# Kernel tuning notes

Measured on AMD Instinct MI355X. Metric: run time of the kernel, lower is better.

The kernel has to match this reference:

```python
import jax, jax.numpy as jnp
import numpy as np

B, L, C, H, D2 = 1, 384, 256, 8, 128
d = C // H
EPS = 1e-5
SCALE = 1.0 / np.sqrt(d).astype(np.float32)


def setup_inputs() -> dict:
    key = jax.random.key(0)
    ks = jax.random.split(key, 20)

    def lin(k, fin, fout):
        return (jax.random.normal(k, (fin, fout), jnp.float32) / np.sqrt(fin)).astype(jnp.float32)

    return {
        "x2d": jax.random.normal(ks[0], (B, L, L, D2), jnp.float32),
        "x3d": jax.random.normal(ks[1], (B, L, C), jnp.float32),
        "Wq": lin(ks[2], C, C), "bq": jax.random.normal(ks[3], (C,), jnp.float32) * 0.02,
        "Wk": lin(ks[4], C, C), "bk": jax.random.normal(ks[5], (C,), jnp.float32) * 0.02,
        "Wv": lin(ks[6], C, C), "bv": jax.random.normal(ks[7], (C,), jnp.float32) * 0.02,
        "Wpre": lin(ks[8], D2, C), "bpre": jax.random.normal(ks[9], (C,), jnp.float32) * 0.02,
        "ln_g": jnp.ones((C,), jnp.float32), "ln_b": jnp.zeros((C,), jnp.float32),
        "Weq": lin(ks[10], C, C), "beq": jax.random.normal(ks[11], (C,), jnp.float32) * 0.02,
        "Wek": lin(ks[12], C, C), "bek": jax.random.normal(ks[13], (C,), jnp.float32) * 0.02,
        "Wo": lin(ks[14], C, C), "bo": jax.random.normal(ks[15], (C,), jnp.float32) * 0.02,
    }


def reference(x2d, x3d, Wq, bq, Wk, bk, Wv, bv, Wpre, bpre, ln_g, ln_b,
              Weq, beq, Wek, bek, Wo, bo):
    def heads(x):  # (B,L,C) -> (B,H,L,d)
        return x.reshape(B, L, H, d).transpose(0, 2, 1, 3)

    q = heads(x3d @ Wq + bq)
    k = heads(x3d @ Wk + bk)
    v = heads(x3d @ Wv + bv)

    # pre_proj: Linear -> LayerNorm -> ReLU on pair features
    e = x2d @ Wpre + bpre                              # (B,L,L,C)
    mu = jnp.mean(e, axis=-1, keepdims=True)
    var = jnp.mean((e - mu) ** 2, axis=-1, keepdims=True)
    e = jax.nn.relu((e - mu) * jax.lax.rsqrt(var + EPS) * ln_g + ln_b)

    efq = (e @ Weq + beq).reshape(B, L, L, H, d)       # efq[b,i,j,h,:]
    efk = (e @ Wek + bek).reshape(B, L, L, H, d)

    # scores[b,h,i,j] = q_i.k_j + sum_d efk[b,i,j,h,d]*q[b,h,j,d], then scale
    scores = jnp.einsum('bhid,bhjd->bhij', q, k) \
           + jnp.einsum('bijhd,bhjd->bhij', efk, q)
    scores = scores * SCALE

    w = jax.nn.softmax(scores, axis=-1)
    x1 = jnp.einsum('bhij,bhjd->bhid', w, v)
    # x2[b,h,i,d] = sum_j scores[b,h,i,j] * efq[b,i,j,h,d]
    x2 = jnp.einsum('bhij,bijhd->bhid', scores, efq)

    x = (x1 + x2).transpose(0, 2, 1, 3).reshape(B, L, C)
    return x @ Wo + bo
```

## Files before the change

kernel.cpp:

```cpp
#include <hip/hip_runtime.h>
#include <hip/hip_bf16.h>

#define LLEN 384
#define CDIM 256
#define NH 8
#define HD 32
#define DIN 128
#define LN_EPS 1e-5f
#define SCL 0.17677669529663687f

typedef __attribute__((ext_vector_type(8))) short bh8;
typedef __attribute__((ext_vector_type(4))) float f32x4;
typedef __attribute__((ext_vector_type(4))) unsigned int u32x4;

__device__ __forceinline__ unsigned short f2bf(float f){
  unsigned int u = __float_as_uint(f);
  u += 0x7fffu + ((u >> 16) & 1u);
  return (unsigned short)(u >> 16);
}

__device__ __forceinline__ float pk_reduce8(const float* v, int lane){
  bool b0 = lane & 1, b1 = lane & 2, b2 = lane & 4;
  float r0 = (b0 ? v[1] : v[0]) + __shfl_xor(b0 ? v[0] : v[1], 1, 64);
  float r1 = (b0 ? v[3] : v[2]) + __shfl_xor(b0 ? v[2] : v[3], 1, 64);
  float r2 = (b0 ? v[5] : v[4]) + __shfl_xor(b0 ? v[4] : v[5], 1, 64);
  float r3 = (b0 ? v[7] : v[6]) + __shfl_xor(b0 ? v[6] : v[7], 1, 64);
  float s0 = (b1 ? r1 : r0) + __shfl_xor(b1 ? r0 : r1, 2, 64);
  float s1 = (b1 ? r3 : r2) + __shfl_xor(b1 ? r2 : r3, 2, 64);
  float t0 = (b2 ? s1 : s0) + __shfl_xor(b2 ? s0 : s1, 4, 64);
  return t0 + __shfl_xor(t0, 8, 64);
}

__global__ __launch_bounds__(256) void pack_w(
    const float* __restrict__ Wpre, const float* __restrict__ Weq,
    const float* __restrict__ Wek,  const float* __restrict__ Wq,
    const float* __restrict__ Wk,   const float* __restrict__ Wv,
    unsigned short* __restrict__ Pp, unsigned short* __restrict__ Pq,
    unsigned short* __restrict__ Pk, unsigned short* __restrict__ PWq,
    unsigned short* __restrict__ PWk, unsigned short* __restrict__ PWv)
{
  int tid = blockIdx.x * 256 + threadIdx.x;
  const float* W; unsigned short* P; int base;
  if      (tid <  4096){ W = Wpre; P = Pp;  base = tid;         }
  else if (tid < 12288){ W = Weq;  P = Pq;  base = tid -  4096; }
  else if (tid < 20480){ W = Wek;  P = Pk;  base = tid - 12288; }
  else if (tid < 28672){ W = Wq;   P = PWq; base = tid - 20480; }
  else if (tid < 36864){ W = Wk;   P = PWk; base = tid - 28672; }
  else                 { W = Wv;   P = PWv; base = tid - 36864; }
  int l   = base & 63;
  int c   = (base >> 6) & 15;
  int kc  = base >> 10;
  int krow = kc*32 + (l >> 4)*8;
  int col  = c*16 + (l & 15);
  unsigned int wds[4];
  #pragma unroll
  for (int p = 0; p < 4; p++){
    unsigned short lo = f2bf(W[(size_t)(krow + 2*p    )*CDIM + col]);
    unsigned short hi = f2bf(W[(size_t)(krow + 2*p + 1)*CDIM + col]);
    wds[p] = (unsigned int)lo | ((unsigned int)hi << 16);
  }
  uint4 v; v.x = wds[0]; v.y = wds[1]; v.z = wds[2]; v.w = wds[3];
  *(uint4*)(P + (size_t)base*8) = v;
}

__global__ __launch_bounds__(256) void qkv_mfma(
    const float* __restrict__ x3d,
    const float* __restrict__ bq, const float* __restrict__ bk, const float* __restrict__ bv,
    const unsigned short* __restrict__ PWq, const unsigned short* __restrict__ PWk,
    const unsigned short* __restrict__ PWv,
    float* __restrict__ Vm, unsigned short* __restrict__ QmH,
    float* __restrict__ QmT, unsigned short* __restrict__ PKt)
{
  __shared__ __align__(16) unsigned short Xb[64*264];
  const int bx = blockIdx.x;
  const int jb = bx / 3, m = bx % 3;
  const int t  = threadIdx.x;
  const int w  = t >> 6, l = t & 63, q4 = l >> 4, lm = l & 15;
  const int wbase = w << 6;

  const float* src = x3d + (size_t)jb*64*CDIM;
  #pragma unroll
  for (int it = 0; it < 16; it++){
    int idx = it*256 + t;
    int r = idx >> 6, k4 = (idx & 63) << 2;
    float4 v = *(const float4*)(src + (size_t)r*CDIM + k4);
    ushort4 b;
    b.x = f2bf(v.x); b.y = f2bf(v.y); b.z = f2bf(v.z); b.w = f2bf(v.w);
    *(ushort4*)(&Xb[r*264 + k4]) = b;
  }
  __syncthreads();

  const unsigned short* P = (m == 0) ? PWq : (m == 1) ? PWk : PWv;
  const float* bias       = (m == 0) ? bq  : (m == 1) ? bk  : bv;
  f32x4 acc[4][4];
  #pragma unroll
  for (int a = 0; a < 4; a++)
    #pragma unroll
    for (int b = 0; b < 4; b++){ f32x4 z = {0.f,0.f,0.f,0.f}; acc[a][b] = z; }
  #pragma unroll
  for (int kc = 0; kc < 8; kc++){
    bh8 af[4];
    #pragma unroll
    for (int rt = 0; rt < 4; rt++)
      af[rt] = *(const bh8*)(&Xb[(rt*16 + lm)*264 + kc*32 + q4*8]);
    #pragma unroll
    for (int ct = 0; ct < 4; ct++){
      bh8 bf = *(const bh8*)(P + ((size_t)(kc*16 + (w*4 + ct))*64 + l)*8);
      #pragma unroll
      for (int rt = 0; rt < 4; rt++)
        acc[rt][ct] = __builtin_amdgcn_mfma_f32_16x16x32_bf16(af[rt], bf, acc[rt][ct], 0, 0, 0);
    }
  }
  #pragma unroll
  for (int ct = 0; ct < 4; ct++){
    int c = wbase + ct*16 + lm;
    float bb = bias[c];
    #pragma unroll
    for (int rt = 0; rt < 4; rt++)
      #pragma unroll
      for (int rg = 0; rg < 4; rg++){
        int row = jb*64 + rt*16 + q4*4 + rg;
        float v = acc[rt][ct][rg] + bb;
        if (m == 0){
          QmH[(size_t)row*CDIM + c] = f2bf(v);
          QmT[(size_t)c*LLEN + row] = v;
        } else if (m == 1){
          int kc2 = c >> 5;
          int jj2 = c & 7;
          int l2  = ((c >> 3) & 3)*16 + (row & 15);
          PKt[(((size_t)kc2*24 + (row >> 4))*64 + l2)*8 + jj2] = f2bf(v);
        } else {
          Vm[(size_t)row*CDIM + c] = v;
        }
      }
  }
}

__global__ __launch_bounds__(256, 3) void x3d_tiles(
  const float* __restrict__ x2d,
  const float* __restrict__ bpre, const float* __restrict__ ln_g, const float* __restrict__ ln_b,
  const float* __restrict__ beq,  const float* __restrict__ bek,
  const float* __restrict__ QmT,  const unsigned short* __restrict__ QmH,
  const unsigned short* __restrict__ PKt,
  const unsigned short* __restrict__ Pp, const unsigned short* __restrict__ Pq,
  const unsigned short* __restrict__ Pk,
  float* __restrict__ Sg, float* __restrict__ x2part)
{
  __shared__ __align__(16) unsigned short EX[64*264];
  __shared__ float rowstat[4][64][2];
  __shared__ float muS[64], istdS[64];
  __shared__ float bpreS[CDIM], gS[CDIM], bSh[CDIM], beqS[CDIM], bekS[CDIM];
  __shared__ float qk1S[NH*64];

  const int bx = blockIdx.x;
  const int i = bx / 6, jt = bx % 6, j0 = jt * 64;
  const int t = threadIdx.x;
  const int w = t >> 6, l = t & 63, q4 = l >> 4, lm = l & 15;
  const int wbase = w << 6;

  {
    #pragma unroll
    for (int hh = 0; hh < 2; hh++){
      int h = 2*w + hh;
      bh8 aq = *(const bh8*)(QmH + (size_t)i*CDIM + h*HD + q4*8);
      #pragma unroll
      for (int ct = 0; ct < 4; ct++){
        bh8 bf = *(const bh8*)(PKt + (((size_t)h*24 + (jt*4 + ct))*64 + l)*8);
        f32x4 z = {0.f,0.f,0.f,0.f};
        f32x4 a1 = __builtin_amdgcn_mfma_f32_16x16x32_bf16(aq, bf, z, 0, 0, 0);
        if (q4 == 0) qk1S[h*64 + ct*16 + lm] = a1[0];
      }
    }
  }

  bpreS[t] = bpre[t]; gS[t] = ln_g[t]; bSh[t] = ln_b[t];
  beqS[t]  = beq[t];  bekS[t] = bek[t];

  {
    const float* src = x2d + ((size_t)i*LLEN + j0)*DIN;
    #pragma unroll
    for (int it = 0; it < 8; it++){
      int r  = it*8 + (t >> 5);
      int k4 = (t & 31)*4;
      u32x4 uv = __builtin_nontemporal_load((const u32x4*)(src + (size_t)r*DIN + k4));
      ushort4 b;
      b.x = f2bf(__uint_as_float(uv.x)); b.y = f2bf(__uint_as_float(uv.y));
      b.z = f2bf(__uint_as_float(uv.z)); b.w = f2bf(__uint_as_float(uv.w));
      *(ushort4*)(&EX[r*136 + k4]) = b;
    }
  }
  __syncthreads();

  f32x4 acc[4][4];
  #pragma unroll
  for (int a = 0; a < 4; a++)
    #pragma unroll
    for (int b = 0; b < 4; b++){ f32x4 z = {0.f,0.f,0.f,0.f}; acc[a][b] = z; }
  #pragma unroll
  for (int kc = 0; kc < 4; kc++){
    bh8 af[4];
    #pragma unroll
    for (int rt = 0; rt < 4; rt++)
      af[rt] = *(const bh8*)(&EX[(rt*16 + lm)*136 + kc*32 + q4*8]);
    #pragma unroll
    for (int ct = 0; ct < 4; ct++){
      bh8 bf = *(const bh8*)(Pp + ((size_t)(kc*16 + (w*4 + ct))*64 + l)*8);
      #pragma unroll
      for (int rt = 0; rt < 4; rt++)
        acc[rt][ct] = __builtin_amdgcn_mfma_f32_16x16x32_bf16(af[rt], bf, acc[rt][ct], 0, 0, 0);
    }
  }

  #pragma unroll
  for (int rt = 0; rt < 4; rt++){
    float v[8];
    #pragma unroll
    for (int p = 0; p < 8; p++) v[p] = 0.f;
    #pragma unroll
    for (int ct = 0; ct < 4; ct++){
      float bb = bpreS[wbase + ct*16 + lm];
      #pragma unroll
      for (int rg = 0; rg < 4; rg++){
        float x = acc[rt][ct][rg] + bb;
        acc[rt][ct][rg] = x;
        v[2*rg]   += x;
        v[2*rg+1] += x*x;
      }
    }
    float red = pk_reduce8(v, lm);
    if (lm < 8){
      int p = lm;
      rowstat[w][rt*16 + q4*4 + (p >> 1)][p & 1] = red;
    }
  }
  __syncthreads();
  if (t < 64){
    float s  = rowstat[0][t][0] + rowstat[1][t][0] + rowstat[2][t][0] + rowstat[3][t][0];
    float s2 = rowstat[0][t][1] + rowstat[1][t][1] + rowstat[2][t][1] + rowstat[3][t][1];
    float mu = s * (1.f/256.f);
    float var = s2 * (1.f/256.f) - mu*mu;
    muS[t] = mu;
    istdS[t] = rsqrtf(var + LN_EPS);
  }
  __syncthreads();

  #pragma unroll
  for (int rt = 0; rt < 4; rt++){
    #pragma unroll
    for (int rg = 0; rg < 4; rg++){
      int row = rt*16 + q4*4 + rg;
      float mu = muS[row], is = istdS[row];
      #pragma unroll
      for (int ct = 0; ct < 4; ct++){
        int c = wbase + ct*16 + lm;
        float v = (acc[rt][ct][rg] - mu)*is*gS[c] + bSh[c];
        v = fmaxf(v, 0.f);
        EX[row*264 + c] = f2bf(v);
      }
    }
  }
  __syncthreads();

  #pragma unroll
  for (int a = 0; a < 4; a++)
    #pragma unroll
    for (int b = 0; b < 4; b++){ f32x4 z = {0.f,0.f,0.f,0.f}; acc[a][b] = z; }
  #pragma unroll
  for (int kc = 0; kc < 8; kc++){
    bh8 af[4];
    #pragma unroll
    for (int rt = 0; rt < 4; rt++)
      af[rt] = *(const bh8*)(&EX[(rt*16 + lm)*264 + kc*32 + q4*8]);
    #pragma unroll
    for (int ct = 0; ct < 4; ct++){
      bh8 bf = *(const bh8*)(Pk + ((size_t)(kc*16 + (w*4 + ct))*64 + l)*8);
      #pragma unroll
      for (int rt = 0; rt < 4; rt++)
        acc[rt][ct] = __builtin_amdgcn_mfma_f32_16x16x32_bf16(af[rt], bf, acc[rt][ct], 0, 0, 0);
    }
  }

  float screg[4];
  #pragma unroll
  for (int rt = 0; rt < 4; rt++){
    float v[8];
    #pragma unroll
    for (int p = 0; p < 8; p++) v[p] = 0.f;
    #pragma unroll
    for (int ct = 0; ct < 4; ct++){
      int c = wbase + ct*16 + lm;
      float bek_ = bekS[c];
      float4 qv = *(const float4*)(QmT + (size_t)c*LLEN + j0 + rt*16 + q4*4);
      int wh = ct >> 1;
      v[0 + wh] += (acc[rt][ct][0] + bek_) * qv.x;
      v[2 + wh] += (acc[rt][ct][1] + bek_) * qv.y;
      v[4 + wh] += (acc[rt][ct][2] + bek_) * qv.z;
      v[6 + wh] += (acc[rt][ct][3] + bek_) * qv.w;
    }
    float red = pk_reduce8(v, lm);
    int p = lm & 7;
    int jloc = rt*16 + q4*4 + (p >> 1);
    float sc = (red + qk1S[(2*w + (p & 1))*64 + jloc]) * SCL;
    screg[rt] = sc;
    if (lm < 8)
      Sg[((size_t)i*NH + 2*w + (p & 1))*LLEN + j0 + jloc] = sc;
  }

  #pragma unroll
  for (int a = 0; a < 4; a++)
    #pragma unroll
    for (int b = 0; b < 4; b++){ f32x4 z = {0.f,0.f,0.f,0.f}; acc[a][b] = z; }
  #pragma unroll
  for (int kc = 0; kc < 8; kc++){
    bh8 af[4];
    #pragma unroll
    for (int rt = 0; rt < 4; rt++)
      af[rt] = *(const bh8*)(&EX[(rt*16 + lm)*264 + kc*32 + q4*8]);
    #pragma unroll
    for (int ct = 0; ct < 4; ct++){
      bh8 bf = *(const bh8*)(Pq + ((size_t)(kc*16 + (w*4 + ct))*64 + l)*8);
      #pragma unroll
      for (int rt = 0; rt < 4; rt++)
        acc[rt][ct] = __builtin_amdgcn_mfma_f32_16x16x32_bf16(af[rt], bf, acc[rt][ct], 0, 0, 0);
    }
  }

  float x2p[4] = {0.f, 0.f, 0.f, 0.f};
  float bq4[4];
  #pragma unroll
  for (int ct = 0; ct < 4; ct++) bq4[ct] = beqS[wbase + ct*16 + lm];
  #pragma unroll
  for (int rt = 0; rt < 4; rt++){
    float sb[8];
    #pragma unroll
    for (int p = 0; p < 8; p++)
      sb[p] = __shfl(screg[rt], (l & 48) | p, 64);
    #pragma unroll
    for (int ct = 0; ct < 4; ct++){
      int wh = ct >> 1;
      #pragma unroll
      for (int rg = 0; rg < 4; rg++)
        x2p[ct] = fmaf(sb[2*rg + wh], acc[rt][ct][rg] + bq4[ct], x2p[ct]);
    }
  }
  {
    bool b4 = l & 16, b5 = l & 32;
    float r0 = (b4 ? x2p[1] : x2p[0]) + __shfl_xor(b4 ? x2p[0] : x2p[1], 16, 64);
    float r1 = (b4 ? x2p[3] : x2p[2]) + __shfl_xor(b4 ? x2p[2] : x2p[3], 16, 64);
    float q  = (b5 ? r1 : r0) + __shfl_xor(b5 ? r0 : r1, 32, 64);
    int ctq = ((l >> 4) & 1) | (((l >> 5) & 1) << 1);
    x2part[((size_t)jt*LLEN + i)*CDIM + wbase + ctq*16 + lm] = q;
  }
}

__global__ __launch_bounds__(256) void finish(
    const float* __restrict__ Sg, const float* __restrict__ x2part,
    const float* __restrict__ Vm, const float* __restrict__ Wo,
    const float* __restrict__ bo, float* __restrict__ out)
{
  __shared__ float scoresS[NH*LLEN];
  __shared__ float xoutS[CDIM];
  const int i = blockIdx.x;
  const int t = threadIdx.x;

  #pragma unroll
  for (int it = 0; it < 3; it++)
    ((float4*)scoresS)[it*256 + t] = ((const float4*)(Sg + (size_t)i*NH*LLEN))[it*256 + t];
  __syncthreads();

  const int h = t >> 5;
  const int g32 = t & 31;
  float sv[12];
  float mx = -3.0e38f;
  #pragma unroll
  for (int it = 0; it < 12; it++){
    float s = scoresS[h*LLEN + it*32 + g32];
    sv[it] = s;
    mx = fmaxf(mx, s);
  }
  #pragma unroll
  for (int mk = 1; mk < 32; mk <<= 1) mx = fmaxf(mx, __shfl_xor(mx, mk, 64));
  float den = 0.f;
  #pragma unroll
  for (int it = 0; it < 12; it++){ float e = __expf(sv[it] - mx); sv[it] = e; den += e; }
  #pragma unroll
  for (int mk = 1; mk < 32; mk <<= 1) den += __shfl_xor(den, mk, 64);
  float rden = 1.f / den;
  #pragma unroll
  for (int it = 0; it < 12; it++) scoresS[h*LLEN + it*32 + g32] = sv[it]*rden;
  __syncthreads();

  float a0 = 0.f, a1 = 0.f, a2 = 0.f, a3 = 0.f;
  {
    const float* vp = Vm + t;
    const float* sp = scoresS + h*LLEN;
    #pragma unroll 4
    for (int j = 0; j < LLEN; j += 4){
      a0 = fmaf(sp[j+0], vp[(size_t)(j+0)*CDIM], a0);
      a1 = fmaf(sp[j+1], vp[(size_t)(j+1)*CDIM], a1);
      a2 = fmaf(sp[j+2], vp[(size_t)(j+2)*CDIM], a2);
      a3 = fmaf(sp[j+3], vp[(size_t)(j+3)*CDIM], a3);
    }
  }
  float x2v = 0.f;
  #pragma unroll
  for (int jt = 0; jt < 6; jt++)
    x2v += x2part[((size_t)jt*LLEN + i)*CDIM + t];
  xoutS[t] = (a0 + a1) + (a2 + a3) + x2v;
  __syncthreads();

  float b0a = bo[t], b1a = 0.f, b2a = 0.f, b3a = 0.f;
  #pragma unroll 4
  for (int c = 0; c < CDIM; c += 4){
    b0a = fmaf(xoutS[c+0], Wo[(size_t)(c+0)*CDIM + t], b0a);
    b1a = fmaf(xoutS[c+1], Wo[(size_t)(c+1)*CDIM + t], b1a);
    b2a = fmaf(xoutS[c+2], Wo[(size_t)(c+2)*CDIM + t], b2a);
    b3a = fmaf(xoutS[c+3], Wo[(size_t)(c+3)*CDIM + t], b3a);
  }
  out[(size_t)i*CDIM + t] = (b0a + b1a) + (b2a + b3a);
}

extern "C" void kernel_launch(void* const* d_in, const int* in_sizes, int n_in,
                              void* d_out, int out_size, void* d_ws, size_t ws_size,
                              hipStream_t stream)
{
  const float* x2d  = (const float*)d_in[0];
  const float* x3d  = (const float*)d_in[1];
  const float* Wq   = (const float*)d_in[2];
  const float* bq   = (const float*)d_in[3];
  const float* Wk   = (const float*)d_in[4];
  const float* bk   = (const float*)d_in[5];
  const float* Wv   = (const float*)d_in[6];
  const float* bv   = (const float*)d_in[7];
  const float* Wpre = (const float*)d_in[8];
  const float* bpre = (const float*)d_in[9];
  const float* ln_g = (const float*)d_in[10];
  const float* ln_b = (const float*)d_in[11];
  const float* Weq  = (const float*)d_in[12];
  const float* beq  = (const float*)d_in[13];
  const float* Wek  = (const float*)d_in[14];
  const float* bek  = (const float*)d_in[15];
  const float* Wo   = (const float*)d_in[16];
  const float* bo   = (const float*)d_in[17];
  float* out = (float*)d_out;

  float* Vm  = (float*)d_ws;
  float* QmT = Vm + LLEN*CDIM;
  unsigned short* QmH = (unsigned short*)(QmT + CDIM*LLEN);
  unsigned short* PKt = QmH + LLEN*CDIM;
  unsigned short* Pp  = PKt + LLEN*CDIM;
  unsigned short* Pq  = Pp  + DIN*CDIM;
  unsigned short* Pk  = Pq  + CDIM*CDIM;
  unsigned short* PWq = Pk  + CDIM*CDIM;
  unsigned short* PWk = PWq + CDIM*CDIM;
  unsigned short* PWv = PWk + CDIM*CDIM;
  float* Sg     = (float*)(PWv + CDIM*CDIM);
  float* x2part = Sg + (size_t)LLEN*NH*LLEN;

  pack_w<<<dim3(176), dim3(256), 0, stream>>>(Wpre, Weq, Wek, Wq, Wk, Wv,
                                              Pp, Pq, Pk, PWq, PWk, PWv);
  qkv_mfma<<<dim3(18), dim3(256), 0, stream>>>(x3d, bq, bk, bv, PWq, PWk, PWv,
                                               Vm, QmH, QmT, PKt);
  x3d_tiles<<<dim3(LLEN*6), dim3(256), 0, stream>>>(x2d, bpre, ln_g, ln_b, beq, bek,
                                                    QmT, QmH, PKt, Pp, Pq, Pk, Sg, x2part);
  finish<<<dim3(LLEN), dim3(256), 0, stream>>>(Sg, x2part, Vm, Wo, bo, out);
}
```

Before: 239.2 us.

## Transpose MFMA operand roles in tile kernel and use packed bf16 conversion

The pre-projection and efk GEMMs in the main tile kernel now put weights in the A slot and activations in the B slot, so each lane holds four consecutive channels per row. This lets LayerNorm stats, bias, gamma/beta and Q loads be vectorized and reduced with fewer cross-lane shuffles. Q is stored row-major instead of transposed, and bias vectors are read straight from global memory instead of being staged in shared memory. The shared-memory cut allows raising the occupancy hint from 3 to 4 blocks. A hardware packed bf16 conversion replaces manual rounding when it is available. The risks are higher register pressure under the tighter launch bound and uncoalesced 4-channel stores into the LDS tile.

Result: no change. 241.8 us (+1.1%).

```diff
diff --git a/kernel.cpp b/kernel.cpp
--- a/kernel.cpp
+++ b/kernel.cpp
@@ -19,16 +19,14 @@
   return (unsigned short)(u >> 16);
 }
 
-__device__ __forceinline__ float pk_reduce8(const float* v, int lane){
-  bool b0 = lane & 1, b1 = lane & 2, b2 = lane & 4;
-  float r0 = (b0 ? v[1] : v[0]) + __shfl_xor(b0 ? v[0] : v[1], 1, 64);
-  float r1 = (b0 ? v[3] : v[2]) + __shfl_xor(b0 ? v[2] : v[3], 1, 64);
-  float r2 = (b0 ? v[5] : v[4]) + __shfl_xor(b0 ? v[4] : v[5], 1, 64);
-  float r3 = (b0 ? v[7] : v[6]) + __shfl_xor(b0 ? v[6] : v[7], 1, 64);
-  float s0 = (b1 ? r1 : r0) + __shfl_xor(b1 ? r0 : r1, 2, 64);
-  float s1 = (b1 ? r3 : r2) + __shfl_xor(b1 ? r2 : r3, 2, 64);
-  float t0 = (b2 ? s1 : s0) + __shfl_xor(b2 ? s0 : s1, 4, 64);
-  return t0 + __shfl_xor(t0, 8, 64);
+__device__ __forceinline__ unsigned int pkbf(float a, float b){
+#if defined(__gfx950__) && __has_builtin(__builtin_amdgcn_cvt_pk_bf16_f32)
+  typedef __attribute__((ext_vector_type(2))) __bf16 vbf2;
+  vbf2 v = __builtin_amdgcn_cvt_pk_bf16_f32(a, b);
+  union { vbf2 v; unsigned int u; } cv; cv.v = v; return cv.u;
+#else
+  return (unsigned int)f2bf(a) | ((unsigned int)f2bf(b) << 16);
+#endif
 }
 
 __global__ __launch_bounds__(256) void pack_w(
@@ -69,7 +67,7 @@
     const unsigned short* __restrict__ PWq, const unsigned short* __restrict__ PWk,
     const unsigned short* __restrict__ PWv,
     float* __restrict__ Vm, unsigned short* __restrict__ QmH,
-    float* __restrict__ QmT, unsigned short* __restrict__ PKt)
+    float* __restrict__ Qm, unsigned short* __restrict__ PKt)
 {
   __shared__ __align__(16) unsigned short Xb[64*264];
   const int bx = blockIdx.x;
@@ -83,10 +81,10 @@
   for (int it = 0; it < 16; it++){
     int idx = it*256 + t;
     int r = idx >> 6, k4 = (idx & 63) << 2;
-    float4 v = *(const float4*)(src + (size_t)r*CDIM + k4);
-    ushort4 b;
-    b.x = f2bf(v.x); b.y = f2bf(v.y); b.z = f2bf(v.z); b.w = f2bf(v.w);
-    *(ushort4*)(&Xb[r*264 + k4]) = b;
+    f32x4 v = *(const f32x4*)(src + (size_t)r*CDIM + k4);
+    unsigned int p0 = pkbf(v[0], v[1]), p1 = pkbf(v[2], v[3]);
+    uint2 pk; pk.x = p0; pk.y = p1;
+    *(uint2*)(&Xb[r*264 + k4]) = pk;
   }
   __syncthreads();
 
@@ -122,8 +120,8 @@
         int row = jb*64 + rt*16 + q4*4 + rg;
         float v = acc[rt][ct][rg] + bb;
         if (m == 0){
+          Qm[(size_t)row*CDIM + c] = v;
           QmH[(size_t)row*CDIM + c] = f2bf(v);
-          QmT[(size_t)c*LLEN + row] = v;
         } else if (m == 1){
           int kc2 = c >> 5;
           int jj2 = c & 7;
@@ -136,11 +134,11 @@
   }
 }
 
-__global__ __launch_bounds__(256, 3) void x3d_tiles(
+__global__ __launch_bounds__(256, 4) void x3d_tiles(
   const float* __restrict__ x2d,
   const float* __restrict__ bpre, const float* __restrict__ ln_g, const float* __restrict__ ln_b,
   const float* __restrict__ beq,  const float* __restrict__ bek,
-  const float* __restrict__ QmT,  const unsigned short* __restrict__ QmH,
+  const float* __restrict__ Qm,   const unsigned short* __restrict__ QmH,
   const unsigned short* __restrict__ PKt,
   const unsigned short* __restrict__ Pp, const unsigned short* __restrict__ Pq,
   const unsigned short* __restrict__ Pk,
@@ -149,32 +147,27 @@
   __shared__ __align__(16) unsigned short EX[64*264];
   __shared__ float rowstat[4][64][2];
   __shared__ float muS[64], istdS[64];
-  __shared__ float bpreS[CDIM], gS[CDIM], bSh[CDIM], beqS[CDIM], bekS[CDIM];
-  __shared__ float qk1S[NH*64];
+  __shared__ __align__(16) float scoresS[NH*64];
 
   const int bx = blockIdx.x;
   const int i = bx / 6, jt = bx % 6, j0 = jt * 64;
   const int t = threadIdx.x;
   const int w = t >> 6, l = t & 63, q4 = l >> 4, lm = l & 15;
   const int wbase = w << 6;
-
-  {
-    #pragma unroll
-    for (int hh = 0; hh < 2; hh++){
-      int h = 2*w + hh;
-      bh8 aq = *(const bh8*)(QmH + (size_t)i*CDIM + h*HD + q4*8);
-      #pragma unroll
-      for (int ct = 0; ct < 4; ct++){
-        bh8 bf = *(const bh8*)(PKt + (((size_t)h*24 + (jt*4 + ct))*64 + l)*8);
-        f32x4 z = {0.f,0.f,0.f,0.f};
-        f32x4 a1 = __builtin_amdgcn_mfma_f32_16x16x32_bf16(aq, bf, z, 0, 0, 0);
-        if (q4 == 0) qk1S[h*64 + ct*16 + lm] = a1[0];
-      }
-    }
-  }
-
-  bpreS[t] = bpre[t]; gS[t] = ln_g[t]; bSh[t] = ln_b[t];
-  beqS[t]  = beq[t];  bekS[t] = bek[t];
+  const bool b4 = l & 16, b5 = l & 32;
+
+  #pragma unroll
+  for (int hh = 0; hh < 2; hh++){
+    int h = 2*w + hh;
+    bh8 aq = *(const bh8*)(QmH + (size_t)i*CDIM + h*HD + q4*8);
+    #pragma unroll
+    for (int ct = 0; ct < 4; ct++){
+      bh8 bf = *(const bh8*)(PKt + (((size_t)h*24 + (jt*4 + ct))*64 + l)*8);
+      f32x4 z = {0.f,0.f,0.f,0.f};
+      f32x4 a1 = __builtin_amdgcn_mfma_f32_16x16x32_bf16(aq, bf, z, 0, 0, 0);
+      if (q4 == 0) scoresS[h*64 + ct*16 + lm] = a1[0];
+    }
+  }
 
   {
     const float* src = x2d + ((size_t)i*LLEN + j0)*DIN;
@@ -183,10 +176,10 @@
       int r  = it*8 + (t >> 5);
       int k4 = (t & 31)*4;
       u32x4 uv = __builtin_nontemporal_load((const u32x4*)(src + (size_t)r*DIN + k4));
-      ushort4 b;
-      b.x = f2bf(__uint_as_float(uv.x)); b.y = f2bf(__uint_as_float(uv.y));
-      b.z = f2bf(__uint_as_float(uv.z)); b.w = f2bf(__uint_as_float(uv.w));
-      *(ushort4*)(&EX[r*136 + k4]) = b;
+      uint2 pk;
+      pk.x = pkbf(__uint_as_float(uv.x), __uint_as_float(uv.y));
+      pk.y = pkbf(__uint_as_float(uv.z), __uint_as_float(uv.w));
+      *(uint2*)(&EX[r*136 + k4]) = pk;
     }
   }
   __syncthreads();
@@ -198,40 +191,44 @@
     for (int b = 0; b < 4; b++){ f32x4 z = {0.f,0.f,0.f,0.f}; acc[a][b] = z; }
   #pragma unroll
   for (int kc = 0; kc < 4; kc++){
-    bh8 af[4];
-    #pragma unroll
-    for (int rt = 0; rt < 4; rt++)
-      af[rt] = *(const bh8*)(&EX[(rt*16 + lm)*136 + kc*32 + q4*8]);
-    #pragma unroll
-    for (int ct = 0; ct < 4; ct++){
-      bh8 bf = *(const bh8*)(Pp + ((size_t)(kc*16 + (w*4 + ct))*64 + l)*8);
-      #pragma unroll
-      for (int rt = 0; rt < 4; rt++)
-        acc[rt][ct] = __builtin_amdgcn_mfma_f32_16x16x32_bf16(af[rt], bf, acc[rt][ct], 0, 0, 0);
-    }
-  }
-
-  #pragma unroll
-  for (int rt = 0; rt < 4; rt++){
-    float v[8];
-    #pragma unroll
-    for (int p = 0; p < 8; p++) v[p] = 0.f;
-    #pragma unroll
-    for (int ct = 0; ct < 4; ct++){
-      float bb = bpreS[wbase + ct*16 + lm];
-      #pragma unroll
-      for (int rg = 0; rg < 4; rg++){
-        float x = acc[rt][ct][rg] + bb;
-        acc[rt][ct][rg] = x;
-        v[2*rg]   += x;
-        v[2*rg+1] += x*x;
-      }
-    }
-    float red = pk_reduce8(v, lm);
-    if (lm < 8){
-      int p = lm;
-      rowstat[w][rt*16 + q4*4 + (p >> 1)][p & 1] = red;
-    }
+    bh8 xf[4];
+    #pragma unroll
+    for (int nt = 0; nt < 4; nt++)
+      xf[nt] = *(const bh8*)(&EX[(nt*16 + lm)*136 + kc*32 + q4*8]);
+    #pragma unroll
+    for (int mt = 0; mt < 4; mt++){
+      bh8 wf = *(const bh8*)(Pp + ((size_t)(kc*16 + (w*4 + mt))*64 + l)*8);
+      #pragma unroll
+      for (int nt = 0; nt < 4; nt++)
+        acc[mt][nt] = __builtin_amdgcn_mfma_f32_16x16x32_bf16(wf, xf[nt], acc[mt][nt], 0, 0, 0);
+    }
+  }
+
+  {
+    float vs[4] = {0,0,0,0}, vq[4] = {0,0,0,0};
+    #pragma unroll
+    for (int mt = 0; mt < 4; mt++){
+      int cb = wbase + mt*16 + q4*4;
+      f32x4 bp = *(const f32x4*)(bpre + cb);
+      #pragma unroll
+      for (int nt = 0; nt < 4; nt++)
+        #pragma unroll
+        for (int rg = 0; rg < 4; rg++){
+          float x = acc[mt][nt][rg] + bp[rg];
+          acc[mt][nt][rg] = x;
+          vs[nt] += x; vq[nt] += x*x;
+        }
+    }
+    float r0 = (b4 ? vs[1] : vs[0]) + __shfl_xor(b4 ? vs[0] : vs[1], 16, 64);
+    float r1 = (b4 ? vs[3] : vs[2]) + __shfl_xor(b4 ? vs[2] : vs[3], 16, 64);
+    float ssum = (b5 ? r1 : r0) + __shfl_xor(b5 ? r0 : r1, 32, 64);
+    float u0 = (b4 ? vq[1] : vq[0]) + __shfl_xor(b4 ? vq[0] : vq[1], 16, 64);
+    float u1 = (b4 ? vq[3] : vq[2]) + __shfl_xor(b4 ? vq[2] : vq[3], 16, 64);
+    float ssq = (b5 ? u1 : u0) + __shfl_xor(b5 ? u0 : u1, 32, 64);
+    int ntl = (b5 ? 2 : 0) + (b4 ? 1 : 0);
+    int jl = ntl*16 + lm;
+    rowstat[w][jl][0] = ssum;
+    rowstat[w][jl][1] = ssq;
   }
   __syncthreads();
   if (t < 64){
@@ -244,22 +241,79 @@
   }
   __syncthreads();
 
-  #pragma unroll
-  for (int rt = 0; rt < 4; rt++){
-    #pragma unroll
-    for (int rg = 0; rg < 4; rg++){
-      int row = rt*16 + q4*4 + rg;
-      float mu = muS[row], is = istdS[row];
-      #pragma unroll
-      for (int ct = 0; ct < 4; ct++){
-        int c = wbase + ct*16 + lm;
-        float v = (acc[rt][ct][rg] - mu)*is*gS[c] + bSh[c];
-        v = fmaxf(v, 0.f);
-        EX[row*264 + c] = f2bf(v);
+  {
+    float muL[4], isL[4];
+    #pragma unroll
+    for (int nt = 0; nt < 4; nt++){
+      muL[nt] = muS[nt*16 + lm];
+      isL[nt] = istdS[nt*16 + lm];
+    }
+    #pragma unroll
+    for (int mt = 0; mt < 4; mt++){
+      int cb = wbase + mt*16 + q4*4;
+      f32x4 g4 = *(const f32x4*)(ln_g + cb);
+      f32x4 bb4 = *(const f32x4*)(ln_b + cb);
+      #pragma unroll
+      for (int nt = 0; nt < 4; nt++){
+        float e0 = fmaxf((acc[mt][nt][0] - muL[nt])*isL[nt]*g4[0] + bb4[0], 0.f);
+        float e1 = fmaxf((acc[mt][nt][1] - muL[nt])*isL[nt]*g4[1] + bb4[1], 0.f);
+        float e2 = fmaxf((acc[mt][nt][2] - muL[nt])*isL[nt]*g4[2] + bb4[2], 0.f);
+        float e3 = fmaxf((acc[mt][nt][3] - muL[nt])*isL[nt]*g4[3] + bb4[3], 0.f);
+        uint2 pk; pk.x = pkbf(e0, e1); pk.y = pkbf(e2, e3);
+        *(uint2*)(&EX[(nt*16 + lm)*264 + cb]) = pk;
       }
     }
   }
   __syncthreads();
+
+  #pragma unroll
+  for (int a = 0; a < 4; a++)
+    #pragma unroll
+    for (int b = 0; b < 4; b++){ f32x4 z = {0.f,0.f,0.f,0.f}; acc[a][b] = z; }
+  #pragma unroll
+  for (int kc = 0; kc < 8; kc++){
+    bh8 xf[4];
+    #pragma unroll
+    for (int nt = 0; nt < 4; nt++)
+      xf[nt] = *(const bh8*)(&EX[(nt*16 + lm)*264 + kc*32 + q4*8]);
+    #pragma unroll
+    for (int mt = 0; mt < 4; mt++){
+      bh8 wf = *(const bh8*)(Pk + ((size_t)(kc*16 + (w*4 + mt))*64 + l)*8);
+      #pragma unroll
+      for (int nt = 0; nt < 4; nt++)
+        acc[mt][nt] = __builtin_amdgcn_mfma_f32_16x16x32_bf16(wf, xf[nt], acc[mt][nt], 0, 0, 0);
+    }
+  }
+
+  {
+    f32x4 bk4[4];
+    #pragma unroll
+    for (int mt = 0; mt < 4; mt++)
+      bk4[mt] = *(const f32x4*)(bek + wbase + mt*16 + q4*4);
+    #pragma unroll
+    for (int nt = 0; nt < 4; nt++){
+      int j = nt*16 + lm;
+      float v0 = 0.f, v1 = 0.f;
+      #pragma unroll
+      for (int mt = 0; mt < 4; mt++){
+        int cb = wbase + mt*16 + q4*4;
+        f32x4 qv = *(const f32x4*)(Qm + (size_t)(j0 + j)*CDIM + cb);
+        float p = (acc[mt][nt][0] + bk4[mt][0]) * qv[0]
+                + (acc[mt][nt][1] + bk4[mt][1]) * qv[1]
+                + (acc[mt][nt][2] + bk4[mt][2]) * qv[2]
+                + (acc[mt][nt][3] + bk4[mt][3]) * qv[3];
+        if (mt < 2) v0 += p; else v1 += p;
+      }
+      float r = (b4 ? v1 : v0) + __shfl_xor(b4 ? v0 : v1, 16, 64);
+      float s = r + __shfl_xor(r, 32, 64);
+      int h = 2*w + (b4 ? 1 : 0);
+      float sc = (s + scoresS[h*64 + j]) * SCL;
+      if (!b5){
+        scoresS[h*64 + j] = sc;
+        Sg[((size_t)i*NH + h)*LLEN + j0 + j] = sc;
+      }
+    }
+  }
 
   #pragma unroll
   for (int a = 0; a < 4; a++)
@@ -273,82 +327,34 @@
       af[rt] = *(const bh8*)(&EX[(rt*16 + lm)*264 + kc*32 + q4*8]);
     #pragma unroll
     for (int ct = 0; ct < 4; ct++){
-      bh8 bf = *(const bh8*)(Pk + ((size_t)(kc*16 + (w*4 + ct))*64 + l)*8);
+      bh8 bf = *(const bh8*)(Pq + ((size_t)(kc*16 + (w*4 + ct))*64 + l)*8);
       #pragma unroll
       for (int rt = 0; rt < 4; rt++)
         acc[rt][ct] = __builtin_amdgcn_mfma_f32_16x16x32_bf16(af[rt], bf, acc[rt][ct], 0, 0, 0);
     }
   }
 
-  float screg[4];
-  #pragma unroll
-  for (int rt = 0; rt < 4; rt++){
-    float v[8];
-    #pragma unroll
-    for (int p = 0; p < 8; p++) v[p] = 0.f;
-    #pragma unroll
-    for (int ct = 0; ct < 4; ct++){
-      int c = wbase + ct*16 + lm;
-      float bek_ = bekS[c];
-      float4 qv = *(const float4*)(QmT + (size_t)c*LLEN + j0 + rt*16 + q4*4);
-      int wh = ct >> 1;
-      v[0 + wh] += (acc[rt][ct][0] + bek_) * qv.x;
-      v[2 + wh] += (acc[rt][ct][1] + bek_) * qv.y;
-      v[4 + wh] += (acc[rt][ct][2] + bek_) * qv.z;
-      v[6 + wh] += (acc[rt][ct][3] + bek_) * qv.w;
-    }
-    float red = pk_reduce8(v, lm);
-    int p = lm & 7;
-    int jloc = rt*16 + q4*4 + (p >> 1);
-    float sc = (red + qk1S[(2*w + (p & 1))*64 + jloc]) * SCL;
-    screg[rt] = sc;
-    if (lm < 8)
-      Sg[((size_t)i*NH + 2*w + (p & 1))*LLEN + j0 + jloc] = sc;
-  }
-
-  #pragma unroll
-  for (int a = 0; a < 4; a++)
-    #pragma unroll
-    for (int b = 0; b < 4; b++){ f32x4 z = {0.f,0.f,0.f,0.f}; acc[a][b] = z; }
-  #pragma unroll
-  for (int kc = 0; kc < 8; kc++){
-    bh8 af[4];
-    #pragma unroll
-    for (int rt = 0; rt < 4; rt++)
-      af[rt] = *(const bh8*)(&EX[(rt*16 + lm)*264 + kc*32 + q4*8]);
-    #pragma unroll
-    for (int ct = 0; ct < 4; ct++){
-      bh8 bf = *(const bh8*)(Pq + ((size_t)(kc*16 + (w*4 + ct))*64 + l)*8);
-      #pragma unroll
-      for (int rt = 0; rt < 4; rt++)
-        acc[rt][ct] = __builtin_amdgcn_mfma_f32_16x16x32_bf16(af[rt], bf, acc[rt][ct], 0, 0, 0);
-    }
-  }
-
-  float x2p[4] = {0.f, 0.f, 0.f, 0.f};
-  float bq4[4];
-  #pragma unroll
-  for (int ct = 0; ct < 4; ct++) bq4[ct] = beqS[wbase + ct*16 + lm];
-  #pragma unroll
-  for (int rt = 0; rt < 4; rt++){
-    float sb[8];
-    #pragma unroll
-    for (int p = 0; p < 8; p++)
-      sb[p] = __shfl(screg[rt], (l & 48) | p, 64);
-    #pragma unroll
-    for (int ct = 0; ct < 4; ct++){
-      int wh = ct >> 1;
-      #pragma unroll
-      for (int rg = 0; rg < 4; rg++)
-        x2p[ct] = fmaf(sb[2*rg + wh], acc[rt][ct][rg] + bq4[ct], x2p[ct]);
-    }
-  }
-  {
-    bool b4 = l & 16, b5 = l & 32;
+  {
+    float bq4[4];
+    #pragma unroll
+    for (int ct = 0; ct < 4; ct++) bq4[ct] = beq[wbase + ct*16 + lm];
+    float x2p[4] = {0.f, 0.f, 0.f, 0.f};
+    #pragma unroll
+    for (int rt = 0; rt < 4; rt++){
+      f32x4 s0 = *(const f32x4*)(&scoresS[(2*w    )*64 + rt*16 + q4*4]);
+      f32x4 s1 = *(const f32x4*)(&scoresS[(2*w + 1)*64 + rt*16 + q4*4]);
+      #pragma unroll
+      for (int ct = 0; ct < 4; ct++){
+        const f32x4& sv = (ct < 2) ? s0 : s1;
+        #pragma unroll
+        for (int rg = 0; rg < 4; rg++)
+          x2p[ct] = fmaf(sv[rg], acc[rt][ct][rg] + bq4[ct], x2p[ct]);
+      }
+    }
     float r0 = (b4 ? x2p[1] : x2p[0]) + __shfl_xor(b4 ? x2p[0] : x2p[1], 16, 64);
     float r1 = (b4 ? x2p[3] : x2p[2]) + __shfl_xor(b4 ? x2p[2] : x2p[3], 16, 64);
     float q  = (b5 ? r1 : r0) + __shfl_xor(b5 ? r0 : r1, 32, 64);
-    int ctq = ((l >> 4) & 1) | (((l >> 5) & 1) << 1);
+    int ctq = (b4 ? 1 : 0) | (b5 ? 2 : 0);
     x2part[((size_t)jt*LLEN + i)*CDIM + wbase + ctq*16 + lm] = q;
   }
 }
@@ -444,9 +450,9 @@
   const float* bo   = (const float*)d_in[17];
   float* out = (float*)d_out;
 
-  float* Vm  = (float*)d_ws;
-  float* QmT = Vm + LLEN*CDIM;
-  unsigned short* QmH = (unsigned short*)(QmT + CDIM*LLEN);
+  float* Vm = (float*)d_ws;
+  float* Qm = Vm + LLEN*CDIM;
+  unsigned short* QmH = (unsigned short*)(Qm + LLEN*CDIM);
   unsigned short* PKt = QmH + LLEN*CDIM;
   unsigned short* Pp  = PKt + LLEN*CDIM;
   unsigned short* Pq  = Pp  + DIN*CDIM;
@@ -460,8 +466,8 @@
   pack_w<<<dim3(176), dim3(256), 0, stream>>>(Wpre, Weq, Wek, Wq, Wk, Wv,
                                               Pp, Pq, Pk, PWq, PWk, PWv);
   qkv_mfma<<<dim3(18), dim3(256), 0, stream>>>(x3d, bq, bk, bv, PWq, PWk, PWv,
-                                               Vm, QmH, QmT, PKt);
+                                               Vm, QmH, Qm, PKt);
   x3d_tiles<<<dim3(LLEN*6), dim3(256), 0, stream>>>(x2d, bpre, ln_g, ln_b, beq, bek,
-                                                    QmT, QmH, PKt, Pp, Pq, Pk, Sg, x2part);
+                                                    Qm, QmH, PKt, Pp, Pq, Pk, Sg, x2part);
   finish<<<dim3(LLEN), dim3(256), 0, stream>>>(Sg, x2part, Vm, Wo, bo, out);
 }
```
